# Kernel optimization log

Measured on AMD Instinct MI355X. Metric: run time of the kernel, lower is better.

Reference implementation:

```python
import jax, jax.numpy as jnp
import numpy as np

B, S, D, H, L, NITEMS = 512, 200, 64, 2, 2, 100000
HD = D // H
EPS = 1e-8
C = 0.001


def _ln(x, w, b):
    m = jnp.mean(x, -1, keepdims=True)
    v = jnp.mean((x - m) ** 2, -1, keepdims=True)
    return (x - m) / jnp.sqrt(v + EPS) * w + b


def _frob(x):
    return jnp.sqrt(jnp.sum(x * x))


def setup_inputs() -> dict:
    key = jax.random.key(0)
    ks = jax.random.split(key, 20)
    rn = lambda k, shape, s=0.02: jax.random.normal(k, shape, jnp.float32) * s
    item_emb = rn(ks[0], (NITEMS + 1, D))
    pos_emb = rn(ks[1], (S + 1, D)).at[0].set(0.0)  # padding_idx=0 row
    pred_w = rn(ks[2], (1, D))
    inp = {
        'user_ids': jax.random.randint(ks[3], (B,), 0, NITEMS, dtype=jnp.int32),
        'log_seqs': jax.random.randint(ks[4], (B, S), 0, NITEMS + 1, dtype=jnp.int32),
        'pos_seqs': jax.random.randint(ks[5], (B, S), 0, NITEMS + 1, dtype=jnp.int32),
        'item_emb': item_emb, 'pos_emb': pos_emb, 'pred_w': pred_w,
        'ln_w': jnp.ones((L, D), jnp.float32), 'ln_b': rn(ks[6], (L, D)),
        'qkv_w': rn(ks[7], (L, 3 * D, D)), 'qkv_b': rn(ks[8], (L, 3 * D)),
        'out_w': rn(ks[9], (L, D, D)), 'out_b': rn(ks[10], (L, D)),
        'fc1_w': rn(ks[11], (L, D, D)), 'fc1_b': rn(ks[12], (L, D)),
        'ffln_w': jnp.ones((L, D), jnp.float32), 'ffln_b': rn(ks[13], (L, D)),
        'fc2_w': rn(ks[14], (L, D, D)), 'fc2_b': rn(ks[15], (L, D)),
        'ffln2_w': jnp.ones((L, D), jnp.float32), 'ffln2_b': rn(ks[16], (L, D)),
    }
    return inp


def reference(user_ids, log_seqs, pos_seqs, item_emb, pos_emb, pred_w,
              ln_w, ln_b, qkv_w, qkv_b, out_w, out_b,
              fc1_w, fc1_b, ffln_w, ffln_b, fc2_w, fc2_b, ffln2_w, ffln2_b):
    # ---- log2feats ----
    x = item_emb[log_seqs] * jnp.sqrt(jnp.float32(D))  # (B,S,D)
    poss = jnp.arange(1, S + 1, dtype=log_seqs.dtype)[None, :] * (log_seqs != 0)
    x = x + pos_emb[poss]
    causal_bias = jnp.where(jnp.tril(jnp.ones((S, S), bool)), 0.0, -1e30).astype(jnp.float32)
    for l in range(L):
        q_in = _ln(x, ln_w[l], ln_b[l])  # query uses pre-LN, K/V use raw seqs
        q = (q_in @ qkv_w[l, :D].T + qkv_b[l, :D]).reshape(B, S, H, HD)
        k = (x @ qkv_w[l, D:2 * D].T + qkv_b[l, D:2 * D]).reshape(B, S, H, HD)
        v = (x @ qkv_w[l, 2 * D:].T + qkv_b[l, 2 * D:]).reshape(B, S, H, HD)
        sc = jnp.einsum('bqhd,bkhd->bhqk', q, k) / jnp.sqrt(jnp.float32(HD)) + causal_bias
        a = jax.nn.softmax(sc, -1)
        ctx = jnp.einsum('bhqk,bkhd->bqhd', a, v).reshape(B, S, D)
        x = q_in + ctx @ out_w[l].T + out_b[l]
        h = jax.nn.relu(_ln(x, ffln_w[l], ffln_b[l]) @ fc1_w[l].T + fc1_b[l])
        x = h @ fc2_w[l].T + fc2_b[l] + _ln(x, ffln2_w[l], ffln2_b[l])
    # ---- left(): quadratic form via Gram matrices (math identical to outer-product sum) ----
    FF = jnp.einsum('bsi,bsj->ij', x, x)          # sum_b F_b^T F_b  (d,d)
    EE = item_emb.T @ item_emb                      # (d,d)
    hh = pred_w.T @ pred_w                          # (d,d)
    left = C * jnp.sum(FF * EE * hh)
    # ---- right() ----
    ps = (x * item_emb[pos_seqs]) @ pred_w[0]       # (B,S), prediction has no bias
    right = jnp.sum((1.0 - C) * ps ** 2 - 2.0 * ps)
    # ---- reg_loss(): sum of per-parameter Frobenius norms ----
    reg = _frob(item_emb) + _frob(pos_emb) + _frob(pred_w)
    for p in (ln_w, ln_b, qkv_w, qkv_b, out_w, out_b, fc1_w, fc1_b,
              ffln_w, ffln_b, fc2_w, fc2_b, ffln2_w, ffln2_b):
        reg = reg + jnp.sum(jax.vmap(_frob)(p))  # per-layer params are separate tensors
    return left + right + 0.1 * reg
```

## Files before the change

kernel.cpp:

```cpp
#include <hip/hip_runtime.h>
#include <math.h>

#define BB 512
#define SS 200
#define DDIM 64
#define HD 32
#define LL 2
#define NROWS (BB * SS)
#define EPS 1e-8f
#define CC 0.001f
#define GRAM_NB 256
#define LSTRIDE 72
#define XS 68
#define QROWS 208

typedef __attribute__((ext_vector_type(8))) short bf16x8;
typedef __attribute__((ext_vector_type(4))) float f32x4;

__device__ unsigned short g_qb[NROWS * DDIM];
__device__ float g_gpart[2 * GRAM_NB * 4096];
__device__ unsigned short g_wb[49152];

__device__ __forceinline__ float wave_sum(float v) {
#pragma unroll
    for (int o = 32; o > 0; o >>= 1) v += __shfl_xor(v, o, 64);
    return v;
}
__device__ __forceinline__ unsigned short f2b(float f) {
    unsigned u = __float_as_uint(f);
    return (unsigned short)((u + 0x7FFFu + ((u >> 16) & 1u)) >> 16);
}

__global__ __launch_bounds__(256) void prep_weights(const float* __restrict__ qkv_w,
                                                    const float* __restrict__ out_w,
                                                    const float* __restrict__ fc1_w,
                                                    const float* __restrict__ fc2_w,
                                                    unsigned short* __restrict__ wb) {
    int i4 = (blockIdx.x * 256 + threadIdx.x) * 4;
    const float* src; int off;
    if (i4 < 24576)      { src = qkv_w; off = 0; }
    else if (i4 < 32768) { src = out_w; off = 24576; }
    else if (i4 < 40960) { src = fc1_w; off = 32768; }
    else                 { src = fc2_w; off = 40960; }
    float4 f = *(const float4*)&src[i4 - off];
    ushort4 o; o.x = f2b(f.x); o.y = f2b(f.y); o.z = f2b(f.z); o.w = f2b(f.w);
    *(ushort4*)&wb[i4] = o;
}

__device__ __forceinline__ bf16x8 frag_raw(const float* Xf, int row, int c0) {
    const float* p = &Xf[row * XS + c0];
    float4 u = *(const float4*)p;
    float4 v = *(const float4*)(p + 4);
    bf16x8 r;
    r[0] = (short)f2b(u.x); r[1] = (short)f2b(u.y); r[2] = (short)f2b(u.z); r[3] = (short)f2b(u.w);
    r[4] = (short)f2b(v.x); r[5] = (short)f2b(v.y); r[6] = (short)f2b(v.z); r[7] = (short)f2b(v.w);
    return r;
}
__device__ __forceinline__ bf16x8 frag_ln(const float* Xf, const float* stats,
                                          const float* vw, const float* vb,
                                          int row, int c0) {
    float m = stats[row * 2], rs = stats[row * 2 + 1];
    const float* p = &Xf[row * XS + c0];
    float4 u = *(const float4*)p;
    float4 v = *(const float4*)(p + 4);
    bf16x8 r;
    r[0] = (short)f2b((u.x - m) * rs * vw[c0 + 0] + vb[c0 + 0]);
    r[1] = (short)f2b((u.y - m) * rs * vw[c0 + 1] + vb[c0 + 1]);
    r[2] = (short)f2b((u.z - m) * rs * vw[c0 + 2] + vb[c0 + 2]);
    r[3] = (short)f2b((u.w - m) * rs * vw[c0 + 3] + vb[c0 + 3]);
    r[4] = (short)f2b((v.x - m) * rs * vw[c0 + 4] + vb[c0 + 4]);
    r[5] = (short)f2b((v.y - m) * rs * vw[c0 + 5] + vb[c0 + 5]);
    r[6] = (short)f2b((v.z - m) * rs * vw[c0 + 6] + vb[c0 + 6]);
    r[7] = (short)f2b((v.w - m) * rs * vw[c0 + 7] + vb[c0 + 7]);
    return r;
}

__device__ __forceinline__ void load_wf(const unsigned short* __restrict__ Wg,
                                        int m16, int quad, bf16x8 wf[8]) {
#pragma unroll
    for (int nt = 0; nt < 4; ++nt) {
        wf[nt * 2]     = *(const bf16x8*)&Wg[(nt * 16 + m16) * 64 + quad * 8];
        wf[nt * 2 + 1] = *(const bf16x8*)&Wg[(nt * 16 + m16) * 64 + 32 + quad * 8];
    }
}
__device__ __forceinline__ void gemm_rw(bf16x8 a0, bf16x8 a1, const bf16x8 wf[8], f32x4 acc[4]) {
#pragma unroll
    for (int nt = 0; nt < 4; ++nt) {
        acc[nt] = __builtin_amdgcn_mfma_f32_16x16x32_bf16(a0, wf[nt * 2], acc[nt], 0, 0, 0);
        acc[nt] = __builtin_amdgcn_mfma_f32_16x16x32_bf16(a1, wf[nt * 2 + 1], acc[nt], 0, 0, 0);
    }
}

__global__ __launch_bounds__(1024)
__attribute__((amdgpu_waves_per_eu(4, 4)))
void mega(const int* __restrict__ log_seqs,
          const int* __restrict__ pos_seqs,
          const float* __restrict__ item_emb,
          const float* __restrict__ pos_emb,
          const float* __restrict__ pred_w,
          const float* __restrict__ ln_w,  const float* __restrict__ ln_b,
          const float* __restrict__ qkv_b,
          const float* __restrict__ out_b,
          const float* __restrict__ fc1_b, const float* __restrict__ fc2_b,
          const float* __restrict__ ffln_w, const float* __restrict__ ffln_b,
          const float* __restrict__ ffln2_w, const float* __restrict__ ffln2_b,
          const unsigned short* __restrict__ wb,
          unsigned short* __restrict__ xb,
          float* __restrict__ rpart) {
    __shared__ float Xf[200 * XS];
    __shared__ unsigned short Qb[QROWS * 72];
    __shared__ unsigned short Kb[QROWS * 72];
    __shared__ unsigned short Vt[64 * 232];
    __shared__ float stats[200 * 2];
    __shared__ float vecs[13][64];
    __shared__ float redw[16];

    const int t = threadIdx.x, b = blockIdx.x;
    const int w = t >> 6, lane = t & 63, m16 = lane & 15, quad = lane >> 4;
    const f32x4 Z = {0.f, 0.f, 0.f, 0.f};

    if (t < 64) vecs[12][t] = pred_w[t];
    if (t < 512) {
        int r2 = t >> 3, cc = 200 + (t & 7) * 4;
        ushort4 z4; z4.x = z4.y = z4.z = z4.w = 0;
        *(ushort4*)&Vt[r2 * 232 + cc] = z4;
    }
    {
        int rr = t >> 2;
        if (rr < 200) {
            int li = log_seqs[b * SS + rr];
            int poss = li ? (rr + 1) : 0;
            int qd = (t & 3) * 16;
            float4 v[4];
#pragma unroll
            for (int g = 0; g < 4; ++g) {
                float4 e = *(const float4*)&item_emb[(long)li * DDIM + qd + g * 4];
                float4 p = *(const float4*)&pos_emb[(long)poss * DDIM + qd + g * 4];
                v[g].x = e.x * 8.0f + p.x; v[g].y = e.y * 8.0f + p.y;
                v[g].z = e.z * 8.0f + p.z; v[g].w = e.w * 8.0f + p.w;
                *(float4*)&Xf[rr * XS + qd + g * 4] = v[g];
            }
            float s1 = 0.f, s2 = 0.f;
#pragma unroll
            for (int g = 0; g < 4; ++g) {
                s1 += (v[g].x + v[g].y) + (v[g].z + v[g].w);
                s2 += (v[g].x * v[g].x + v[g].y * v[g].y) + (v[g].z * v[g].z + v[g].w * v[g].w);
            }
            s1 += __shfl_xor(s1, 1, 64); s1 += __shfl_xor(s1, 2, 64);
            s2 += __shfl_xor(s2, 1, 64); s2 += __shfl_xor(s2, 2, 64);
            float mean = s1 * (1.f / 64.f);
            float var = s2 * (1.f / 64.f) - mean * mean;
            float rs = rsqrtf(var + EPS);
            if ((t & 3) == 0) { stats[rr * 2] = mean; stats[rr * 2 + 1] = rs; }
        }
    }

    for (int l = 0; l < LL; ++l) {
        __syncthreads();
        if (t < 64) {
            vecs[0][t] = qkv_b[l * 192 + t];
            vecs[1][t] = qkv_b[l * 192 + 64 + t];
            vecs[2][t] = qkv_b[l * 192 + 128 + t];
            vecs[3][t] = ln_w[l * 64 + t];   vecs[4][t] = ln_b[l * 64 + t];
            vecs[5][t] = out_b[l * 64 + t];
            vecs[6][t] = fc1_b[l * 64 + t];  vecs[7][t] = fc2_b[l * 64 + t];
            vecs[8][t] = ffln_w[l * 64 + t]; vecs[9][t] = ffln_b[l * 64 + t];
            vecs[10][t] = ffln2_w[l * 64 + t]; vecs[11][t] = ffln2_b[l * 64 + t];
        }
        __syncthreads();
        {
            int gsel, wbase, nwv;
            if (w < 6)       { gsel = 0; wbase = 0;  nwv = 6; }
            else if (w < 11) { gsel = 1; wbase = 6;  nwv = 5; }
            else             { gsel = 2; wbase = 11; nwv = 5; }
            bf16x8 wf[8];
            load_wf(wb + l * 12288 + gsel * 4096, m16, quad, wf);
            const float* bias = vecs[gsel];
            for (int tt = w - wbase; tt < 13; tt += nwv) {
                int tb = tt * 16;
                int row = tb + m16; if (row > 199) row = 199;
                bf16x8 a0, a1;
                if (gsel == 0) {
                    a0 = frag_ln(Xf, stats, vecs[3], vecs[4], row, quad * 8);
                    a1 = frag_ln(Xf, stats, vecs[3], vecs[4], row, 32 + quad * 8);
                } else {
                    a0 = frag_raw(Xf, row, quad * 8);
                    a1 = frag_raw(Xf, row, 32 + quad * 8);
                }
                f32x4 acc[4] = {Z, Z, Z, Z};
                gemm_rw(a0, a1, wf, acc);
#pragma unroll
                for (int nt = 0; nt < 4; ++nt) {
                    int n = nt * 16 + m16; float bbv = bias[n];
#pragma unroll
                    for (int rg = 0; rg < 4; ++rg) {
                        int m = tb + quad * 4 + rg;
                        float val = acc[nt][rg] + bbv;
                        if (gsel == 0)      Qb[m * 72 + n] = f2b(val);
                        else if (gsel == 1) Kb[m * 72 + n] = f2b(val);
                        else if (m < 200)   Vt[n * 232 + m] = f2b(val);
                    }
                }
            }
        }
        __syncthreads();
        {
            const unsigned long long tab0 = 0x01170016FF19FF18ull;
            const unsigned long long tab1 = 0x0513041203150214ull;
            const unsigned long long tab2 = 0x090F080E07110610ull;
            const unsigned long long tab3 = 0xFFFFFFFF0B0D0A0Cull;
            unsigned long long tv = (w & 8) ? ((w & 4) ? tab3 : tab2) : ((w & 4) ? tab1 : tab0);
            unsigned su = (unsigned)((tv >> ((w & 3) * 16)) & 0xFFFFu);
            const float scale = 0.17677669529663687f;
            for (int slot = 0; slot < 2; ++slot) {
                int u = (su >> (slot * 8)) & 0xFF;
                if (u == 0xFF) break;
                int h = u & 1, qt = u >> 1;
                int q0 = qt * 16;
                int qrow = q0 + m16; if (qrow > 199) qrow = 199;
                bf16x8 qa = *(const bf16x8*)&Qb[qrow * 72 + h * 32 + quad * 8];
                __builtin_amdgcn_wave_barrier();
                unsigned short* ps = &Qb[q0 * 72 + h * 32];
                f32x4 o0 = Z, o1 = Z;
                float lsum[4] = {0.f, 0.f, 0.f, 0.f};
                int np = (qt + 2) >> 1;
                for (int pi = 0; pi < np; ++pi) {
                    int p0 = pi * 32;
                    int kr0 = p0 + m16;      int kr0c = kr0 > 199 ? 199 : kr0;
                    int kr1 = p0 + 16 + m16; int kr1c = kr1 > 199 ? 199 : kr1;
                    bf16x8 kb0 = *(const bf16x8*)&Kb[kr0c * 72 + h * 32 + quad * 8];
                    bf16x8 kb1 = *(const bf16x8*)&Kb[kr1c * 72 + h * 32 + quad * 8];
                    f32x4 s0 = __builtin_amdgcn_mfma_f32_16x16x32_bf16(qa, kb0, Z, 0, 0, 0);
                    f32x4 s1 = __builtin_amdgcn_mfma_f32_16x16x32_bf16(qa, kb1, Z, 0, 0, 0);
                    float e0[4], e1[4];
#pragma unroll
                    for (int rg = 0; rg < 4; ++rg) {
                        int rglob = q0 + quad * 4 + rg;
                        e0[rg] = (kr0 <= rglob && kr0 < SS) ? __expf(s0[rg] * scale) : 0.f;
                        e1[rg] = (kr1 <= rglob && kr1 < SS) ? __expf(s1[rg] * scale) : 0.f;
                        lsum[rg] += e0[rg] + e1[rg];
                    }
                    __builtin_amdgcn_wave_barrier();
#pragma unroll
                    for (int rg = 0; rg < 4; ++rg) {
                        int row = quad * 4 + rg;
                        ps[row * 72 + m16] = f2b(e0[rg]);
                        ps[row * 72 + 16 + m16] = f2b(e1[rg]);
                    }
                    __builtin_amdgcn_wave_barrier();
                    bf16x8 pa = *(const bf16x8*)&ps[m16 * 72 + quad * 8];
                    bf16x8 vb0 = *(const bf16x8*)&Vt[(h * 32 + m16) * 232 + p0 + quad * 8];
                    bf16x8 vb1 = *(const bf16x8*)&Vt[(h * 32 + 16 + m16) * 232 + p0 + quad * 8];
                    o0 = __builtin_amdgcn_mfma_f32_16x16x32_bf16(pa, vb0, o0, 0, 0, 0);
                    o1 = __builtin_amdgcn_mfma_f32_16x16x32_bf16(pa, vb1, o1, 0, 0, 0);
                }
#pragma unroll
                for (int rg = 0; rg < 4; ++rg)
#pragma unroll
                    for (int o = 1; o <= 8; o <<= 1) lsum[rg] += __shfl_xor(lsum[rg], o, 64);
                __builtin_amdgcn_wave_barrier();
#pragma unroll
                for (int rg = 0; rg < 4; ++rg) {
                    int rglob = q0 + quad * 4 + rg;
                    if (rglob < SS) {
                        float inv = 1.f / lsum[rg];
                        Qb[rglob * 72 + h * 32 + m16] = f2b(o0[rg] * inv);
                        Qb[rglob * 72 + h * 32 + 16 + m16] = f2b(o1[rg] * inv);
                    }
                }
            }
        }
        __syncthreads();
        if (w < 13) {
            int tb = w * 16;
            bf16x8 wf[8];
            load_wf(wb + 24576 + l * 4096, m16, quad, wf);
            int row = tb + m16; if (row > 199) row = 199;
            bf16x8 a0 = *(const bf16x8*)&Qb[row * 72 + quad * 8];
            bf16x8 a1 = *(const bf16x8*)&Qb[row * 72 + 32 + quad * 8];
            f32x4 acc1[4] = {Z, Z, Z, Z};
            gemm_rw(a0, a1, wf, acc1);
            float core[4][4];
#pragma unroll
            for (int nt = 0; nt < 4; ++nt) {
                int n = nt * 16 + m16;
                float bbv = vecs[5][n], lw = vecs[3][n], lb = vecs[4][n];
#pragma unroll
                for (int rg = 0; rg < 4; ++rg) {
                    int m = tb + quad * 4 + rg; int mc = m > 199 ? 199 : m;
                    float qin = (Xf[mc * XS + n] - stats[mc * 2]) * stats[mc * 2 + 1] * lw + lb;
                    core[nt][rg] = acc1[nt][rg] + bbv + qin;
                }
            }
#pragma unroll
            for (int rg = 0; rg < 4; ++rg) {
                float s1 = (core[0][rg] + core[1][rg]) + (core[2][rg] + core[3][rg]);
                float s2 = core[0][rg] * core[0][rg] + core[1][rg] * core[1][rg]
                         + core[2][rg] * core[2][rg] + core[3][rg] * core[3][rg];
#pragma unroll
                for (int o = 1; o <= 8; o <<= 1) { s1 += __shfl_xor(s1, o, 64); s2 += __shfl_xor(s2, o, 64); }
                float mean = s1 * (1.f / 64.f);
                float var = s2 * (1.f / 64.f) - mean * mean;
                float rs = rsqrtf(var + EPS);
#pragma unroll
                for (int nt = 0; nt < 4; ++nt) core[nt][rg] = (core[nt][rg] - mean) * rs;
            }
            __builtin_amdgcn_wave_barrier();
#pragma unroll
            for (int nt = 0; nt < 4; ++nt) {
                int n = nt * 16 + m16;
                float w8v = vecs[8][n], b9v = vecs[9][n];
#pragma unroll
                for (int rg = 0; rg < 4; ++rg)
                    Kb[(tb + quad * 4 + rg) * 72 + n] = f2b(core[nt][rg] * w8v + b9v);
            }
            __builtin_amdgcn_wave_barrier();
            load_wf(wb + 32768 + l * 4096, m16, quad, wf);
            a0 = *(const bf16x8*)&Kb[(tb + m16) * 72 + quad * 8];
            a1 = *(const bf16x8*)&Kb[(tb + m16) * 72 + 32 + quad * 8];
            f32x4 acc2[4] = {Z, Z, Z, Z};
            gemm_rw(a0, a1, wf, acc2);
            __builtin_amdgcn_wave_barrier();
#pragma unroll
            for (int nt = 0; nt < 4; ++nt) {
                int n = nt * 16 + m16; float bbv = vecs[6][n];
#pragma unroll
                for (int rg = 0; rg < 4; ++rg)
                    Kb[(tb + quad * 4 + rg) * 72 + n] = f2b(fmaxf(acc2[nt][rg] + bbv, 0.f));
            }
            __builtin_amdgcn_wave_barrier();
            load_wf(wb + 40960 + l * 4096, m16, quad, wf);
            a0 = *(const bf16x8*)&Kb[(tb + m16) * 72 + quad * 8];
            a1 = *(const bf16x8*)&Kb[(tb + m16) * 72 + 32 + quad * 8];
            f32x4 acc3[4] = {Z, Z, Z, Z};
            gemm_rw(a0, a1, wf, acc3);
            float xn[4][4];
#pragma unroll
            for (int nt = 0; nt < 4; ++nt) {
                int n = nt * 16 + m16;
                float bbv = vecs[7][n], lw = vecs[10][n], lb = vecs[11][n];
#pragma unroll
                for (int rg = 0; rg < 4; ++rg)
                    xn[nt][rg] = acc3[nt][rg] + bbv + core[nt][rg] * lw + lb;
            }
#pragma unroll
            for (int rg = 0; rg < 4; ++rg) {
                float s1 = (xn[0][rg] + xn[1][rg]) + (xn[2][rg] + xn[3][rg]);
                float s2 = xn[0][rg] * xn[0][rg] + xn[1][rg] * xn[1][rg]
                         + xn[2][rg] * xn[2][rg] + xn[3][rg] * xn[3][rg];
#pragma unroll
                for (int o = 1; o <= 8; o <<= 1) { s1 += __shfl_xor(s1, o, 64); s2 += __shfl_xor(s2, o, 64); }
                float mean = s1 * (1.f / 64.f);
                float var = s2 * (1.f / 64.f) - mean * mean;
                float rs = rsqrtf(var + EPS);
                int m = tb + quad * 4 + rg;
                if (m < 200) {
#pragma unroll
                    for (int nt = 0; nt < 4; ++nt) Xf[m * XS + nt * 16 + m16] = xn[nt][rg];
                    if (m16 == 0) { stats[m * 2] = mean; stats[m * 2 + 1] = rs; }
                }
            }
        }
    }
    __syncthreads();

    for (int i = t; i < 3200; i += 1024) {
        int r = i >> 4, c4 = (i & 15) * 4;
        float4 f = *(const float4*)&Xf[r * XS + c4];
        ushort4 o; o.x = f2b(f.x); o.y = f2b(f.y); o.z = f2b(f.z); o.w = f2b(f.w);
        *(ushort4*)&xb[((long)b * SS + r) * DDIM + c4] = o;
    }
    float local = 0.f;
    {
        int rr = t >> 2;
        if (rr < 200) {
            int pi = pos_seqs[b * SS + rr];
            int qd = (t & 3) * 16;
            float v = 0.f;
#pragma unroll
            for (int g = 0; g < 4; ++g) {
                float4 xv = *(const float4*)&Xf[rr * XS + qd + g * 4];
                float4 iv = *(const float4*)&item_emb[(long)pi * DDIM + qd + g * 4];
                const float* pwp = &vecs[12][qd + g * 4];
                v += xv.x * iv.x * pwp[0] + xv.y * iv.y * pwp[1]
                   + xv.z * iv.z * pwp[2] + xv.w * iv.w * pwp[3];
            }
            v += __shfl_xor(v, 1, 64); v += __shfl_xor(v, 2, 64);
            if ((t & 3) == 0) local += (1.0f - CC) * v * v - 2.0f * v;
        }
    }
    local = wave_sum(local);
    if (lane == 0) redw[w] = local;
    __syncthreads();
    if (t == 0) {
        float s = 0.f;
#pragma unroll
        for (int i = 0; i < 16; ++i) s += redw[i];
        rpart[b] = s;
    }
}

__global__ __launch_bounds__(256) void gram_kernel(const float* __restrict__ A0, int n0,
                                                   const unsigned short* __restrict__ A1, int n1,
                                                   float* __restrict__ part) {
    __shared__ unsigned short At[64 * LSTRIDE];
    int t = threadIdx.x;
    int second = blockIdx.x >= GRAM_NB;
    int bid = second ? blockIdx.x - GRAM_NB : blockIdx.x;
    int nrows = second ? n1 : n0;
    int w16 = (t >> 6) * 16, lane = t & 63, m16 = lane & 15, quad = lane >> 4;
    int bi = t & 15, bj = t >> 4;
    f32x4 zero = {0.f, 0.f, 0.f, 0.f};
    f32x4 acc[4] = {zero, zero, zero, zero};
    for (long base = (long)bid * 64; base < nrows; base += (long)GRAM_NB * 64) {
        __syncthreads();
        if (!second) {
            float rv[4][4];
#pragma unroll
            for (int e = 0; e < 4; ++e) {
                long gr = base + bj * 4 + e;
                float4 f = make_float4(0.f, 0.f, 0.f, 0.f);
                if (gr < nrows) f = *(const float4*)&A0[gr * DDIM + bi * 4];
                rv[e][0] = f.x; rv[e][1] = f.y; rv[e][2] = f.z; rv[e][3] = f.w;
            }
#pragma unroll
            for (int e = 0; e < 4; ++e) {
                ushort4 o;
                o.x = f2b(rv[0][e]); o.y = f2b(rv[1][e]); o.z = f2b(rv[2][e]); o.w = f2b(rv[3][e]);
                *(ushort4*)&At[(bi * 4 + e) * LSTRIDE + bj * 4] = o;
            }
        } else {
            ushort4 u[4];
#pragma unroll
            for (int e = 0; e < 4; ++e) {
                long gr = base + bj * 4 + e;
                ushort4 uu; uu.x = uu.y = uu.z = uu.w = 0;
                if (gr < nrows) uu = *(const ushort4*)&A1[gr * DDIM + bi * 4];
                u[e] = uu;
            }
#pragma unroll
            for (int e = 0; e < 4; ++e) {
                ushort4 o;
                o.x = ((const unsigned short*)&u[0])[e];
                o.y = ((const unsigned short*)&u[1])[e];
                o.z = ((const unsigned short*)&u[2])[e];
                o.w = ((const unsigned short*)&u[3])[e];
                *(ushort4*)&At[(bi * 4 + e) * LSTRIDE + bj * 4] = o;
            }
        }
        __syncthreads();
#pragma unroll
        for (int ks = 0; ks < 2; ++ks) {
            bf16x8 a = *(const bf16x8*)&At[(w16 + m16) * LSTRIDE + ks * 32 + quad * 8];
#pragma unroll
            for (int nt = 0; nt < 4; ++nt) {
                bf16x8 bfr = *(const bf16x8*)&At[(nt * 16 + m16) * LSTRIDE + ks * 32 + quad * 8];
                acc[nt] = __builtin_amdgcn_mfma_f32_16x16x32_bf16(a, bfr, acc[nt], 0, 0, 0);
            }
        }
    }
    float* slab = part + (long)blockIdx.x * 4096;
#pragma unroll
    for (int nt = 0; nt < 4; ++nt) {
        int n = nt * 16 + m16;
#pragma unroll
        for (int rg = 0; rg < 4; ++rg) {
            int m = w16 + quad * 4 + rg;
            slab[m * 64 + n] = acc[nt][rg];
        }
    }
}

struct NormEntry { const float* p; int n; };
struct NormArgs { NormEntry e[30]; };

__global__ __launch_bounds__(256) void reduce_norms(const float* __restrict__ part,
                                                    float* __restrict__ EE, float* __restrict__ FF,
                                                    NormArgs args, float* __restrict__ norms) {
    __shared__ float red[256];
    int blk = blockIdx.x;
    if (blk < 32) {
        int which = blk >> 4;
        int p = (blk & 15) * 256 + threadIdx.x;
        const float* basep = part + (long)which * GRAM_NB * 4096;
        float s = 0.f;
        for (int b = 0; b < GRAM_NB; ++b) s += basep[(long)b * 4096 + p];
        (which ? FF : EE)[p] = s;
    } else {
        NormEntry en = args.e[blk - 32];
        float s = 0.f;
        for (int i = threadIdx.x; i < en.n; i += 256) { float v = en.p[i]; s += v * v; }
        red[threadIdx.x] = s;
        for (int o = 128; o > 0; o >>= 1) {
            __syncthreads();
            if (threadIdx.x < o) red[threadIdx.x] += red[threadIdx.x + o];
        }
        __syncthreads();
        if (threadIdx.x == 0) norms[blk - 32] = red[0];
    }
}

__global__ __launch_bounds__(256) void final_kernel(const float* __restrict__ EE,
                                                    const float* __restrict__ FF,
                                                    const float* __restrict__ pred_w,
                                                    const float* __restrict__ rpart,
                                                    const float* __restrict__ norms,
                                                    float* __restrict__ out) {
    __shared__ float p_s[64];
    __shared__ float redL[256];
    __shared__ float redT[256];
    __shared__ float redR[256];
    int t = threadIdx.x;
    if (t < 64) p_s[t] = pred_w[t];
    __syncthreads();
    float lf = 0.f, tr = 0.f, rs = 0.f;
    for (int p = t; p < 4096; p += 256) {
        int i = p >> 6, j = p & 63;
        float ee = EE[p];
        lf += FF[p] * ee * p_s[i] * p_s[j];
        if (i == j) tr += ee;
    }
    for (int i = t; i < 512; i += 256) rs += rpart[i];
    redL[t] = lf; redT[t] = tr; redR[t] = rs;
    for (int o = 128; o > 0; o >>= 1) {
        __syncthreads();
        if (t < o) { redL[t] += redL[t + o]; redT[t] += redT[t + o]; redR[t] += redR[t + o]; }
    }
    __syncthreads();
    if (t == 0) {
        float reg = sqrtf(redT[0]);
        for (int s = 0; s < 30; ++s) reg += sqrtf(norms[s]);
        out[0] = CC * redL[0] + redR[0] + 0.1f * reg;
    }
}

struct DevPtrs { float* gpart; unsigned short *qb, *wb; };

static DevPtrs fetch_ptrs() {
    DevPtrs p;
    (void)hipGetSymbolAddress((void**)&p.gpart, HIP_SYMBOL(g_gpart));
    (void)hipGetSymbolAddress((void**)&p.qb,    HIP_SYMBOL(g_qb));
    (void)hipGetSymbolAddress((void**)&p.wb,    HIP_SYMBOL(g_wb));
    return p;
}

extern "C" void kernel_launch(void* const* d_in, const int* in_sizes, int n_in,
                              void* d_out, int out_size, void* d_ws, size_t ws_size,
                              hipStream_t stream) {
    const int*   log_seqs = (const int*)d_in[1];
    const int*   pos_seqs = (const int*)d_in[2];
    const float* item_emb = (const float*)d_in[3];
    const float* pos_emb  = (const float*)d_in[4];
    const float* pred_w   = (const float*)d_in[5];
    const float* ln_w     = (const float*)d_in[6];
    const float* ln_b     = (const float*)d_in[7];
    const float* qkv_w    = (const float*)d_in[8];
    const float* qkv_b    = (const float*)d_in[9];
    const float* out_w    = (const float*)d_in[10];
    const float* out_b    = (const float*)d_in[11];
    const float* fc1_w    = (const float*)d_in[12];
    const float* fc1_b    = (const float*)d_in[13];
    const float* ffln_w   = (const float*)d_in[14];
    const float* ffln_b   = (const float*)d_in[15];
    const float* fc2_w    = (const float*)d_in[16];
    const float* fc2_b    = (const float*)d_in[17];
    const float* ffln2_w  = (const float*)d_in[18];
    const float* ffln2_b  = (const float*)d_in[19];

    static DevPtrs P = fetch_ptrs();

    float* ws    = (float*)d_ws;
    float* rpart = ws;
    float* nrm   = ws + 1664;
    float* EE    = ws + 2048;
    float* FF    = ws + 6144;

    prep_weights<<<48, 256, 0, stream>>>(qkv_w, out_w, fc1_w, fc2_w, P.wb);

    mega<<<BB, 1024, 0, stream>>>(log_seqs, pos_seqs, item_emb, pos_emb, pred_w,
                                  ln_w, ln_b, qkv_b, out_b, fc1_b, fc2_b,
                                  ffln_w, ffln_b, ffln2_w, ffln2_b,
                                  P.wb, P.qb, rpart);

    gram_kernel<<<2 * GRAM_NB, 256, 0, stream>>>(item_emb, 100001, P.qb, NROWS, P.gpart);

    NormArgs na;
    int s = 0;
    na.e[s++] = {pos_emb, (SS + 1) * DDIM};
    na.e[s++] = {pred_w, DDIM};
    for (int l = 0; l < LL; ++l) {
        na.e[s++] = {ln_w + l * 64, 64};
        na.e[s++] = {ln_b + l * 64, 64};
        na.e[s++] = {qkv_w + (long)l * 12288, 12288};
        na.e[s++] = {qkv_b + (long)l * 192, 192};
        na.e[s++] = {out_w + (long)l * 4096, 4096};
        na.e[s++] = {out_b + l * 64, 64};
        na.e[s++] = {fc1_w + (long)l * 4096, 4096};
        na.e[s++] = {fc1_b + l * 64, 64};
        na.e[s++] = {ffln_w + l * 64, 64};
        na.e[s++] = {ffln_b + l * 64, 64};
        na.e[s++] = {fc2_w + (long)l * 4096, 4096};
        na.e[s++] = {fc2_b + l * 64, 64};
        na.e[s++] = {ffln2_w + l * 64, 64};
        na.e[s++] = {ffln2_b + l * 64, 64};
    }
    reduce_norms<<<62, 256, 0, stream>>>(P.gpart, EE, FF, na, nrm);

    final_kernel<<<1, 256, 0, stream>>>(EE, FF, pred_w, rpart, nrm, (float*)d_out);
}
```

Measured before the change: 270.1 us.

## Stage per-GEMM weights in LDS and split QKV projection into sequential phases

Each 64x64 bf16 weight matrix is now copied cooperatively from global memory into a padded shared-memory buffer, and MFMA B-fragments are read from LDS instead of being held in registers loaded per wave. The QKV projection, previously split across wave groups running concurrently, becomes three sequential phases with all 13 waves, each separated by block barriers. The FFN chain is likewise split with block-wide syncs so the shared weight buffer can be reused, and the waves_per_eu attribute is dropped. This reduces redundant global weight loads and register pressure, but adds many __syncthreads and extra LDS traffic.

```diff
diff --git a/kernel.cpp b/kernel.cpp
--- a/kernel.cpp
+++ b/kernel.cpp
@@ -75,24 +75,24 @@
     return r;
 }
 
-__device__ __forceinline__ void load_wf(const unsigned short* __restrict__ Wg,
-                                        int m16, int quad, bf16x8 wf[8]) {
+__device__ __forceinline__ void gemm_lds(bf16x8 a0, bf16x8 a1, const unsigned short* __restrict__ W,
+                                         int m16, int quad, f32x4 acc[4]) {
 #pragma unroll
     for (int nt = 0; nt < 4; ++nt) {
-        wf[nt * 2]     = *(const bf16x8*)&Wg[(nt * 16 + m16) * 64 + quad * 8];
-        wf[nt * 2 + 1] = *(const bf16x8*)&Wg[(nt * 16 + m16) * 64 + 32 + quad * 8];
-    }
-}
-__device__ __forceinline__ void gemm_rw(bf16x8 a0, bf16x8 a1, const bf16x8 wf[8], f32x4 acc[4]) {
-#pragma unroll
-    for (int nt = 0; nt < 4; ++nt) {
-        acc[nt] = __builtin_amdgcn_mfma_f32_16x16x32_bf16(a0, wf[nt * 2], acc[nt], 0, 0, 0);
-        acc[nt] = __builtin_amdgcn_mfma_f32_16x16x32_bf16(a1, wf[nt * 2 + 1], acc[nt], 0, 0, 0);
-    }
+        bf16x8 b0 = *(const bf16x8*)&W[(nt * 16 + m16) * LSTRIDE + quad * 8];
+        bf16x8 b1 = *(const bf16x8*)&W[(nt * 16 + m16) * LSTRIDE + 32 + quad * 8];
+        acc[nt] = __builtin_amdgcn_mfma_f32_16x16x32_bf16(a0, b0, acc[nt], 0, 0, 0);
+        acc[nt] = __builtin_amdgcn_mfma_f32_16x16x32_bf16(a1, b1, acc[nt], 0, 0, 0);
+    }
+}
+
+__device__ __forceinline__ void stage_wb1024(const unsigned short* __restrict__ G,
+                                             unsigned short* __restrict__ L, int t) {
+    int r = t >> 4, c4 = (t & 15) * 4;
+    *(ushort4*)&L[r * LSTRIDE + c4] = *(const ushort4*)&G[r * 64 + c4];
 }
 
 __global__ __launch_bounds__(1024)
-__attribute__((amdgpu_waves_per_eu(4, 4)))
 void mega(const int* __restrict__ log_seqs,
           const int* __restrict__ pos_seqs,
           const float* __restrict__ item_emb,
@@ -111,6 +111,7 @@
     __shared__ unsigned short Qb[QROWS * 72];
     __shared__ unsigned short Kb[QROWS * 72];
     __shared__ unsigned short Vt[64 * 232];
+    __shared__ unsigned short Wb[64 * LSTRIDE];
     __shared__ float stats[200 * 2];
     __shared__ float vecs[13][64];
     __shared__ float redw[16];
@@ -154,9 +155,9 @@
             if ((t & 3) == 0) { stats[rr * 2] = mean; stats[rr * 2 + 1] = rs; }
         }
     }
+    __syncthreads();
 
     for (int l = 0; l < LL; ++l) {
-        __syncthreads();
         if (t < 64) {
             vecs[0][t] = qkv_b[l * 192 + t];
             vecs[1][t] = qkv_b[l * 192 + 64 + t];
@@ -167,39 +168,58 @@
             vecs[8][t] = ffln_w[l * 64 + t]; vecs[9][t] = ffln_b[l * 64 + t];
             vecs[10][t] = ffln2_w[l * 64 + t]; vecs[11][t] = ffln2_b[l * 64 + t];
         }
-        __syncthreads();
-        {
-            int gsel, wbase, nwv;
-            if (w < 6)       { gsel = 0; wbase = 0;  nwv = 6; }
-            else if (w < 11) { gsel = 1; wbase = 6;  nwv = 5; }
-            else             { gsel = 2; wbase = 11; nwv = 5; }
-            bf16x8 wf[8];
-            load_wf(wb + l * 12288 + gsel * 4096, m16, quad, wf);
-            const float* bias = vecs[gsel];
-            for (int tt = w - wbase; tt < 13; tt += nwv) {
-                int tb = tt * 16;
-                int row = tb + m16; if (row > 199) row = 199;
-                bf16x8 a0, a1;
-                if (gsel == 0) {
-                    a0 = frag_ln(Xf, stats, vecs[3], vecs[4], row, quad * 8);
-                    a1 = frag_ln(Xf, stats, vecs[3], vecs[4], row, 32 + quad * 8);
-                } else {
-                    a0 = frag_raw(Xf, row, quad * 8);
-                    a1 = frag_raw(Xf, row, 32 + quad * 8);
-                }
-                f32x4 acc[4] = {Z, Z, Z, Z};
-                gemm_rw(a0, a1, wf, acc);
-#pragma unroll
-                for (int nt = 0; nt < 4; ++nt) {
-                    int n = nt * 16 + m16; float bbv = bias[n];
-#pragma unroll
-                    for (int rg = 0; rg < 4; ++rg) {
-                        int m = tb + quad * 4 + rg;
-                        float val = acc[nt][rg] + bbv;
-                        if (gsel == 0)      Qb[m * 72 + n] = f2b(val);
-                        else if (gsel == 1) Kb[m * 72 + n] = f2b(val);
-                        else if (m < 200)   Vt[n * 232 + m] = f2b(val);
-                    }
+        stage_wb1024(wb + l * 12288, Wb, t);
+        __syncthreads();
+        if (w < 13) {
+            int tb = w * 16;
+            int row = tb + m16; if (row > 199) row = 199;
+            bf16x8 a0 = frag_ln(Xf, stats, vecs[3], vecs[4], row, quad * 8);
+            bf16x8 a1 = frag_ln(Xf, stats, vecs[3], vecs[4], row, 32 + quad * 8);
+            f32x4 acc[4] = {Z, Z, Z, Z};
+            gemm_lds(a0, a1, Wb, m16, quad, acc);
+#pragma unroll
+            for (int nt = 0; nt < 4; ++nt) {
+                int n = nt * 16 + m16; float bbv = vecs[0][n];
+#pragma unroll
+                for (int rg = 0; rg < 4; ++rg)
+                    Qb[(tb + quad * 4 + rg) * 72 + n] = f2b(acc[nt][rg] + bbv);
+            }
+        }
+        __syncthreads();
+        stage_wb1024(wb + l * 12288 + 4096, Wb, t);
+        __syncthreads();
+        if (w < 13) {
+            int tb = w * 16;
+            int row = tb + m16; if (row > 199) row = 199;
+            bf16x8 a0 = frag_raw(Xf, row, quad * 8);
+            bf16x8 a1 = frag_raw(Xf, row, 32 + quad * 8);
+            f32x4 acc[4] = {Z, Z, Z, Z};
+            gemm_lds(a0, a1, Wb, m16, quad, acc);
+#pragma unroll
+            for (int nt = 0; nt < 4; ++nt) {
+                int n = nt * 16 + m16; float bbv = vecs[1][n];
+#pragma unroll
+                for (int rg = 0; rg < 4; ++rg)
+                    Kb[(tb + quad * 4 + rg) * 72 + n] = f2b(acc[nt][rg] + bbv);
+            }
+        }
+        __syncthreads();
+        stage_wb1024(wb + l * 12288 + 8192, Wb, t);
+        __syncthreads();
+        if (w < 13) {
+            int tb = w * 16;
+            int row = tb + m16; if (row > 199) row = 199;
+            bf16x8 a0 = frag_raw(Xf, row, quad * 8);
+            bf16x8 a1 = frag_raw(Xf, row, 32 + quad * 8);
+            f32x4 acc[4] = {Z, Z, Z, Z};
+            gemm_lds(a0, a1, Wb, m16, quad, acc);
+#pragma unroll
+            for (int nt = 0; nt < 4; ++nt) {
+                int n = nt * 16 + m16; float bbv = vecs[2][n];
+#pragma unroll
+                for (int rg = 0; rg < 4; ++rg) {
+                    int m = tb + quad * 4 + rg;
+                    if (m < 200) Vt[n * 232 + m] = f2b(acc[nt][rg] + bbv);
                 }
             }
         }
@@ -271,16 +291,16 @@
             }
         }
         __syncthreads();
+        float core[4][4];
+        stage_wb1024(wb + 24576 + l * 4096, Wb, t);
+        __syncthreads();
         if (w < 13) {
             int tb = w * 16;
-            bf16x8 wf[8];
-            load_wf(wb + 24576 + l * 4096, m16, quad, wf);
             int row = tb + m16; if (row > 199) row = 199;
             bf16x8 a0 = *(const bf16x8*)&Qb[row * 72 + quad * 8];
             bf16x8 a1 = *(const bf16x8*)&Qb[row * 72 + 32 + quad * 8];
             f32x4 acc1[4] = {Z, Z, Z, Z};
-            gemm_rw(a0, a1, wf, acc1);
-            float core[4][4];
+            gemm_lds(a0, a1, Wb, m16, quad, acc1);
 #pragma unroll
             for (int nt = 0; nt < 4; ++nt) {
                 int n = nt * 16 + m16;
@@ -314,12 +334,16 @@
                 for (int rg = 0; rg < 4; ++rg)
                     Kb[(tb + quad * 4 + rg) * 72 + n] = f2b(core[nt][rg] * w8v + b9v);
             }
-            __builtin_amdgcn_wave_barrier();
-            load_wf(wb + 32768 + l * 4096, m16, quad, wf);
-            a0 = *(const bf16x8*)&Kb[(tb + m16) * 72 + quad * 8];
-            a1 = *(const bf16x8*)&Kb[(tb + m16) * 72 + 32 + quad * 8];
+        }
+        __syncthreads();
+        stage_wb1024(wb + 32768 + l * 4096, Wb, t);
+        __syncthreads();
+        if (w < 13) {
+            int tb = w * 16;
+            bf16x8 a0 = *(const bf16x8*)&Kb[(tb + m16) * 72 + quad * 8];
+            bf16x8 a1 = *(const bf16x8*)&Kb[(tb + m16) * 72 + 32 + quad * 8];
             f32x4 acc2[4] = {Z, Z, Z, Z};
-            gemm_rw(a0, a1, wf, acc2);
+            gemm_lds(a0, a1, Wb, m16, quad, acc2);
             __builtin_amdgcn_wave_barrier();
 #pragma unroll
             for (int nt = 0; nt < 4; ++nt) {
@@ -328,12 +352,16 @@
                 for (int rg = 0; rg < 4; ++rg)
                     Kb[(tb + quad * 4 + rg) * 72 + n] = f2b(fmaxf(acc2[nt][rg] + bbv, 0.f));
             }
-            __builtin_amdgcn_wave_barrier();
-            load_wf(wb + 40960 + l * 4096, m16, quad, wf);
-            a0 = *(const bf16x8*)&Kb[(tb + m16) * 72 + quad * 8];
-            a1 = *(const bf16x8*)&Kb[(tb + m16) * 72 + 32 + quad * 8];
+        }
+        __syncthreads();
+        stage_wb1024(wb + 40960 + l * 4096, Wb, t);
+        __syncthreads();
+        if (w < 13) {
+            int tb = w * 16;
+            bf16x8 a0 = *(const bf16x8*)&Kb[(tb + m16) * 72 + quad * 8];
+            bf16x8 a1 = *(const bf16x8*)&Kb[(tb + m16) * 72 + 32 + quad * 8];
             f32x4 acc3[4] = {Z, Z, Z, Z};
-            gemm_rw(a0, a1, wf, acc3);
+            gemm_lds(a0, a1, Wb, m16, quad, acc3);
             float xn[4][4];
 #pragma unroll
             for (int nt = 0; nt < 4; ++nt) {
@@ -361,8 +389,8 @@
                 }
             }
         }
-    }
-    __syncthreads();
+        __syncthreads();
+    }
 
     for (int i = t; i < 3200; i += 1024) {
         int r = i >> 4, c4 = (i & 15) * 4;
```

Measured after the change: 241.2 us. 1.12x faster.
